# Optimization experiments

Measured on AMD Instinct MI355X. Metric: run time of the kernel, lower is better.

The kernel has to match this reference:

```python
import jax, jax.numpy as jnp
import numpy as np

N = 50000      # num nodes
E = 800000     # num edges per edge set (before self loops)
F_IN = 256     # encoding_size
F_EMB = 256    # embedding_size
PE = 98        # d2an positional features (beijing)
ALPHA1 = 0.5
ALPHA2 = 0.5


def _uniform_linear(key, out_f, in_f):
    # torch.nn.Linear default init: U(-1/sqrt(in_f), 1/sqrt(in_f))
    s = 1.0 / np.sqrt(in_f)
    return jax.random.uniform(key, (out_f, in_f), jnp.float32, -s, s)


def setup_inputs() -> dict:
    key = jax.random.key(0)
    ks = jax.random.split(key, 18)
    inp = {
        'x': jax.random.normal(ks[0], (N, F_IN), jnp.float32),
        'd2an': jax.random.normal(ks[1], (N, PE), jnp.float32),
        'edge_index_l0': jax.random.randint(ks[2], (2, E), 0, N, jnp.int32),
        'edge_attr_l0': jax.random.uniform(ks[3], (E,), jnp.float32),
        'edge_index_l1': jax.random.randint(ks[4], (2, E), 0, N, jnp.int32),
        'edge_attr_l1': jax.random.uniform(ks[5], (E,), jnp.float32),
        # nodeLin of conv1/conv2 (used only on firstLayer with usePE)
        'Wnode1': _uniform_linear(ks[6], F_IN, F_IN + PE),
        'Wnode2': _uniform_linear(ks[7], F_IN, F_IN + PE),
        # lin1/lin2 of each conv layer (bias-free linears)
        'W11': _uniform_linear(ks[8], F_EMB, F_IN),
        'W12': _uniform_linear(ks[9], F_EMB, F_IN),
        'W21': _uniform_linear(ks[10], F_EMB, F_IN),
        'W22': _uniform_linear(ks[11], F_EMB, F_IN),
        'W31': _uniform_linear(ks[12], F_EMB, F_EMB),
        'W32': _uniform_linear(ks[13], F_EMB, F_EMB),
        'W41': _uniform_linear(ks[14], F_EMB, F_EMB),
        'W42': _uniform_linear(ks[15], F_EMB, F_EMB),
    }
    return inp


def _pos_knn_gnn_layer(x, row, col, attr, d2an, Wnode, W1, W2, first):
    """PosKnnGNNLayer.forward with useSI=True, usePE=True (eval mode).

    message = deg_norm * (x_j @ W1.T) + edge_norm * (x_j @ W2.T), scatter-add to col.
    Linearity lets us aggregate (norm * x_j) first, then apply W1/W2 once per node.
    """
    n = x.shape[0]
    loop = jnp.arange(n, dtype=row.dtype)
    row = jnp.concatenate([row, loop])          # source j
    col = jnp.concatenate([col, loop])          # target i
    attr = jnp.concatenate([attr, jnp.ones((n,), attr.dtype)])  # self-loop weight 1.0

    if first:
        x = jnp.concatenate([x, d2an], axis=1) @ Wnode.T  # [n, F_IN]

    deg = jax.ops.segment_sum(jnp.ones_like(attr), col, num_segments=n)
    dinv = jnp.where(deg > 0, deg ** -0.5, 0.0)
    deg_norm = dinv[row] * dinv[col]            # [E']

    einv = jnp.where(attr > 0, attr ** -0.5, 0.0)
    edge_norm = jnp.minimum(einv, 1.0)          # clamp values > 1.0 to 1.0

    xj = x[row]                                  # gather [E', F]
    a1 = jax.ops.segment_sum(deg_norm[:, None] * xj, col, num_segments=n)
    a2 = jax.ops.segment_sum(edge_norm[:, None] * xj, col, num_segments=n)
    return a1 @ W1.T + a2 @ W2.T                 # [n, F_EMB]


def reference(x, d2an, edge_index_l0, edge_attr_l0, edge_index_l1, edge_attr_l1,
              Wnode1, Wnode2, W11, W12, W21, W22, W31, W32, W41, W42):
    r0, c0 = edge_index_l0[0], edge_index_l0[1]
    r1, c1 = edge_index_l1[0], edge_index_l1[1]

    x0 = jax.nn.relu(_pos_knn_gnn_layer(x, r0, c0, edge_attr_l0, d2an, Wnode1, W11, W12, True))
    x1 = jax.nn.relu(_pos_knn_gnn_layer(x, r1, c1, edge_attr_l1, d2an, Wnode2, W21, W22, True))
    h = ALPHA1 * x0 + ALPHA2 * x1               # dropout p=0.3 is identity in eval

    x0 = jax.nn.relu(_pos_knn_gnn_layer(h, r0, c0, edge_attr_l0, None, None, W31, W32, False))
    x1 = jax.nn.relu(_pos_knn_gnn_layer(h, r1, c1, edge_attr_l1, None, None, W41, W42, False))
    return ALPHA1 * x0 + ALPHA2 * x1
```

## Files before the change

kernel.cpp:

```cpp
#include <hip/hip_runtime.h>


using bf16x8  = __attribute__((ext_vector_type(8))) __bf16;
using floatx4 = __attribute__((ext_vector_type(4))) float;
using f32x2   = __attribute__((ext_vector_type(2))) float;

__device__ __forceinline__ float b2f(unsigned short b) {
    return __uint_as_float(((unsigned)b) << 16);
}
__device__ __forceinline__ unsigned short f2b(float f) {
    unsigned u = __float_as_uint(f);
    return (unsigned short)((u + 0x7FFFu + ((u >> 16) & 1u)) >> 16);
}
__device__ __forceinline__ unsigned short f2h(float f) {
    _Float16 h = (_Float16)f;
    return __builtin_bit_cast(unsigned short, h);
}
__device__ __forceinline__ float h2f(unsigned short u) {
    return (float)__builtin_bit_cast(_Float16, u);
}


__global__ void k_cnt2(const int* __restrict__ col0, const int* __restrict__ col1,
                       int E, int* __restrict__ cnt0, int* __restrict__ cnt1) {
    int e = blockIdx.x * 256 + threadIdx.x;
    const int* col = blockIdx.y ? col1 : col0;
    int* cnt = blockIdx.y ? cnt1 : cnt0;
    if (e < E) atomicAdd(&cnt[col[e]], 1);
}

__global__ __launch_bounds__(1024) void k_scanA(
    const int* __restrict__ cnt0, const int* __restrict__ cnt1,
    int* __restrict__ off0, int* __restrict__ off1,
    int* __restrict__ bs0, int* __restrict__ bs1, int n) {
    const int* cnt = blockIdx.y ? cnt1 : cnt0;
    int* off = blockIdx.y ? off1 : off0;
    int* bs  = blockIdx.y ? bs1 : bs0;
    __shared__ int wsum[16];
    __shared__ int wpre[16];
    const int t = threadIdx.x;
    const int lane = t & 63;
    const int w = t >> 6;
    const int i = blockIdx.x * 1024 + t;
    int v = (i < n) ? ((cnt[i] + 8) & ~7) : 0;
    #pragma unroll
    for (int d = 1; d < 64; d <<= 1) {
        int u = __shfl_up(v, d, 64);
        if (lane >= d) v += u;
    }
    if (lane == 63) wsum[w] = v;
    __syncthreads();
    if (t < 16) {
        int s2 = wsum[t];
        #pragma unroll
        for (int d = 1; d < 16; d <<= 1) {
            int u = __shfl_up(s2, d, 16);
            if (t >= d) s2 += u;
        }
        wpre[t] = s2;
    }
    __syncthreads();
    int incl = v + (w > 0 ? wpre[w - 1] : 0);
    if (i < n) off[i + 1] = incl;
    if (t == 1023) bs[blockIdx.x] = incl;
}

__global__ void k_scanB(int* __restrict__ bs0, int* __restrict__ bs1, int nb) {
    int* bs = blockIdx.y ? bs1 : bs0;
    const int t = threadIdx.x;
    int v = (t < nb) ? bs[t] : 0;
    int orig = v;
    #pragma unroll
    for (int d = 1; d < 64; d <<= 1) {
        int u = __shfl_up(v, d, 64);
        if (t >= d) v += u;
    }
    if (t < nb) bs[t] = v - orig;
}

__global__ __launch_bounds__(1024) void k_scanC(
    const int* __restrict__ bs0, const int* __restrict__ bs1,
    int* __restrict__ off0, int* __restrict__ off1, int n) {
    int* off = blockIdx.y ? off1 : off0;
    const int* bs = blockIdx.y ? bs1 : bs0;
    const int i = blockIdx.x * 1024 + threadIdx.x;
    if (i == 0) off[0] = 0;
    if (i < n && blockIdx.x > 0) off[i + 1] += bs[blockIdx.x];
}

__global__ void k_prep(const int* __restrict__ cnt0, const int* __restrict__ cnt1,
                       const int* __restrict__ off0, const int* __restrict__ off1,
                       float* __restrict__ dinv0, float* __restrict__ dinv1,
                       int* __restrict__ cur0, int* __restrict__ cur1, int n) {
    int i = blockIdx.x * 256 + threadIdx.x;
    if (i >= n) return;
    const int* cnt = blockIdx.y ? cnt1 : cnt0;
    const int* off = blockIdx.y ? off1 : off0;
    float* dinv = blockIdx.y ? dinv1 : dinv0;
    int* cur = blockIdx.y ? cur1 : cur0;
    dinv[i] = rsqrtf((float)(cnt[i] + 1));
    cur[i] = off[i];
}

__global__ void k_fill2(const int* __restrict__ ei0, const float* __restrict__ ea0,
                        const int* __restrict__ ei1, const float* __restrict__ ea1,
                        int E, const float* __restrict__ dinv0,
                        const float* __restrict__ dinv1,
                        int* __restrict__ cur0, int* __restrict__ cur1,
                        uint2* __restrict__ rec0, uint2* __restrict__ rec1) {
    int e = blockIdx.x * 256 + threadIdx.x;
    if (e >= E) return;
    const int* ei = blockIdx.y ? ei1 : ei0;
    const float* ea = blockIdx.y ? ea1 : ea0;
    const float* dinv = blockIdx.y ? dinv1 : dinv0;
    int* cur = blockIdx.y ? cur1 : cur0;
    uint2* rec = blockIdx.y ? rec1 : rec0;
    int r = ei[e];
    int c = ei[E + e];
    float a = ea[e];
    float w2 = (a > 0.0f) ? fminf(rsqrtf(a), 1.0f) : 0.0f;
    float w1 = dinv[r] * dinv[c];
    int p = atomicAdd(&cur[c], 1);
    rec[p] = make_uint2((unsigned)r,
                        ((unsigned)f2h(w1) << 16) | (unsigned)f2h(w2));
}

__global__ void k_pad(const int* __restrict__ cnt0, const int* __restrict__ cnt1,
                      const int* __restrict__ off0, const int* __restrict__ off1,
                      const float* __restrict__ dinv0, const float* __restrict__ dinv1,
                      uint2* __restrict__ rec0, uint2* __restrict__ rec1, int n) {
    int i = blockIdx.x * 256 + threadIdx.x;
    if (i >= n) return;
    const int* cnt = blockIdx.y ? cnt1 : cnt0;
    const int* off = blockIdx.y ? off1 : off0;
    const float* dinv = blockIdx.y ? dinv1 : dinv0;
    uint2* rec = blockIdx.y ? rec1 : rec0;
    int p = off[i] + cnt[i], pe = off[i + 1];
    float di = dinv[i];
    rec[p++] = make_uint2((unsigned)i,
                          ((unsigned)f2h(di * di) << 16) | 0x3C00u);
    for (; p < pe; ++p) rec[p] = make_uint2(0u, 0u);
}


__global__ void k_xc(const float* __restrict__ x, const float* __restrict__ pe,
                     unsigned short* __restrict__ xc, int n, int F, int PEd,
                     int KC, int KP) {
    int idx = blockIdx.x * 256 + threadIdx.x;
    if (idx >= n * KP) return;
    int i = idx / KP, k = idx - i * KP;
    float v = 0.0f;
    if (k < F)        v = x[(size_t)i * F + k];
    else if (k < KC)  v = pe[(size_t)i * PEd + (k - F)];
    xc[idx] = f2b(v);
}

__global__ void k_wall(const float* __restrict__ Wn1, const float* __restrict__ Wn2,
                       const float* __restrict__ W11, const float* __restrict__ W12,
                       const float* __restrict__ W21, const float* __restrict__ W22,
                       const float* __restrict__ W31, const float* __restrict__ W32,
                       const float* __restrict__ W41, const float* __restrict__ W42,
                       unsigned short* __restrict__ wn0c, unsigned short* __restrict__ wn1c,
                       unsigned short* __restrict__ wc0, unsigned short* __restrict__ wc1,
                       unsigned short* __restrict__ wc2, unsigned short* __restrict__ wc3,
                       int F, int KC, int KP) {
    int idx = blockIdx.x * 256 + threadIdx.x;
    int npad = F * KP;
    if (idx < 2 * npad) {
        const float* W = (idx < npad) ? Wn1 : Wn2;
        unsigned short* Wc = (idx < npad) ? wn0c : wn1c;
        int t = (idx < npad) ? idx : idx - npad;
        int o = t / KP, k = t - o * KP;
        Wc[t] = f2b(k < KC ? W[(size_t)o * KC + k] : 0.0f);
        return;
    }
    int t = idx - 2 * npad;
    int seg = F * 512;
    if (t >= 4 * seg) return;
    int which = t / seg;
    int r = t - which * seg;
    const float* Wa = (which == 0) ? W11 : (which == 1) ? W21 : (which == 2) ? W31 : W41;
    const float* Wb = (which == 0) ? W12 : (which == 1) ? W22 : (which == 2) ? W32 : W42;
    unsigned short* Wc = (which == 0) ? wc0 : (which == 1) ? wc1 : (which == 2) ? wc2 : wc3;
    int o = r >> 9, k = r & 511;
    float v = (k < 256) ? Wa[(size_t)o * 256 + k] : Wb[(size_t)o * 256 + (k - 256)];
    Wc[r] = f2b(v);
}


#define AGG_SLOT(g, wsel)                                                     \
    do {                                                                      \
        float w1 = h2f((unsigned short)((wsel) >> 16));                       \
        float w2 = h2f((unsigned short)((wsel) & 0xFFFFu));                   \
        f32x2 w1v = {w1, w1};                                                 \
        f32x2 w2v = {w2, w2};                                                 \
        f32x2 v;                                                              \
        v.x = __uint_as_float((g).x << 16);                                   \
        v.y = __uint_as_float((g).x & 0xFFFF0000u);                           \
        c1a = __builtin_elementwise_fma(w1v, v, c1a);                         \
        c2a = __builtin_elementwise_fma(w2v, v, c2a);                         \
        v.x = __uint_as_float((g).y << 16);                                   \
        v.y = __uint_as_float((g).y & 0xFFFF0000u);                           \
        c1b = __builtin_elementwise_fma(w1v, v, c1b);                         \
        c2b = __builtin_elementwise_fma(w2v, v, c2b);                         \
        v.x = __uint_as_float((g).z << 16);                                   \
        v.y = __uint_as_float((g).z & 0xFFFF0000u);                           \
        c1c = __builtin_elementwise_fma(w1v, v, c1c);                         \
        c2c = __builtin_elementwise_fma(w2v, v, c2c);                         \
        v.x = __uint_as_float((g).w << 16);                                   \
        v.y = __uint_as_float((g).w & 0xFFFF0000u);                           \
        c1d = __builtin_elementwise_fma(w1v, v, c1d);                         \
        c2d = __builtin_elementwise_fma(w2v, v, c2d);                         \
    } while (0)

__global__ __launch_bounds__(256) void k_agg(
    const unsigned short* __restrict__ X0, const unsigned short* __restrict__ X1,
    const int* __restrict__ off0, const int* __restrict__ off1,
    const uint2* __restrict__ rec0, const uint2* __restrict__ rec1,
    unsigned short* __restrict__ A0, unsigned short* __restrict__ A1, int n) {
    const int s = blockIdx.y;
    const char* Xb = (const char*)(s ? X1 : X0);
    const int* off = s ? off1 : off0;
    const uint2* rec = s ? rec1 : rec0;
    unsigned short* A = s ? A1 : A0;

    const int gw = (blockIdx.x * 256 + threadIdx.x) >> 6;
    const int lane = threadIdx.x & 63;
    if (gw >= n) return;

    const int e0 = __builtin_amdgcn_readfirstlane(off[gw]);
    const int e1 = __builtin_amdgcn_readfirstlane(off[gw + 1]);
    const bool hi = lane >= 32;
    const unsigned loff = (unsigned)(lane & 31) << 4;

    f32x2 c1a = {0.f, 0.f}, c1b = {0.f, 0.f}, c1c = {0.f, 0.f}, c1d = {0.f, 0.f};
    f32x2 c2a = {0.f, 0.f}, c2b = {0.f, 0.f}, c2c = {0.f, 0.f}, c2d = {0.f, 0.f};

    const uint4* recq = (const uint4*)(rec + e0);
    const int nit = (e1 - e0) >> 3;
    for (int it = 0; it < nit; ++it) {
        uint4 qa = recq[it * 4 + 0];
        uint4 qb = recq[it * 4 + 1];
        uint4 qc = recq[it * 4 + 2];
        uint4 qd = recq[it * 4 + 3];
        unsigned sa = hi ? qa.z : qa.x, wa = hi ? qa.w : qa.y;
        unsigned sb = hi ? qb.z : qb.x, wb = hi ? qb.w : qb.y;
        unsigned sc = hi ? qc.z : qc.x, wcs = hi ? qc.w : qc.y;
        unsigned sd = hi ? qd.z : qd.x, wd = hi ? qd.w : qd.y;
        uint4 ga = *(const uint4*)(Xb + ((sa << 9) | loff));
        uint4 gb = *(const uint4*)(Xb + ((sb << 9) | loff));
        uint4 gc = *(const uint4*)(Xb + ((sc << 9) | loff));
        uint4 gd = *(const uint4*)(Xb + ((sd << 9) | loff));
        AGG_SLOT(ga, wa);
        AGG_SLOT(gb, wb);
        AGG_SLOT(gc, wcs);
        AGG_SLOT(gd, wd);
    }

    float u0 = c1a.x + __shfl_xor(c1a.x, 32);
    float u1 = c1a.y + __shfl_xor(c1a.y, 32);
    float u2 = c1b.x + __shfl_xor(c1b.x, 32);
    float u3 = c1b.y + __shfl_xor(c1b.y, 32);
    float u4 = c1c.x + __shfl_xor(c1c.x, 32);
    float u5 = c1c.y + __shfl_xor(c1c.y, 32);
    float u6 = c1d.x + __shfl_xor(c1d.x, 32);
    float u7 = c1d.y + __shfl_xor(c1d.y, 32);
    float t0 = c2a.x + __shfl_xor(c2a.x, 32);
    float t1 = c2a.y + __shfl_xor(c2a.y, 32);
    float t2 = c2b.x + __shfl_xor(c2b.x, 32);
    float t3 = c2b.y + __shfl_xor(c2b.y, 32);
    float t4 = c2c.x + __shfl_xor(c2c.x, 32);
    float t5 = c2c.y + __shfl_xor(c2c.y, 32);
    float t6 = c2d.x + __shfl_xor(c2d.x, 32);
    float t7 = c2d.y + __shfl_xor(c2d.y, 32);

    float s0 = hi ? t0 : u0;
    float s1 = hi ? t1 : u1;
    float s2 = hi ? t2 : u2;
    float s3 = hi ? t3 : u3;
    float s4 = hi ? t4 : u4;
    float s5 = hi ? t5 : u5;
    float s6 = hi ? t6 : u6;
    float s7 = hi ? t7 : u7;
    uint4 o;
    o.x = (unsigned)f2b(s0) | ((unsigned)f2b(s1) << 16);
    o.y = (unsigned)f2b(s2) | ((unsigned)f2b(s3) << 16);
    o.z = (unsigned)f2b(s4) | ((unsigned)f2b(s5) << 16);
    o.w = (unsigned)f2b(s6) | ((unsigned)f2b(s7) << 16);
    *(uint4*)(A + (size_t)gw * 512 + (hi ? 256 : 0) + ((lane & 31) << 3)) = o;
}

#define GLL(g, l) \
    __builtin_amdgcn_global_load_lds((__attribute__((address_space(1))) void*)(g), \
                                     (__attribute__((address_space(3))) void*)(l), 16, 0, 0)

__global__ __launch_bounds__(256) void gemm_bt(
    const unsigned short* __restrict__ A,
    const unsigned short* __restrict__ B0, const unsigned short* __restrict__ B1,
    int M, int K, int Nc,
    unsigned short* __restrict__ outH0, unsigned short* __restrict__ outH1) {
    const unsigned short* B = blockIdx.z ? B1 : B0;
    unsigned short* outH = blockIdx.z ? outH1 : outH0;

    __shared__ __align__(16) unsigned short sA[128 * 32];
    __shared__ __align__(16) unsigned short sB[128 * 32];
    const int tid = threadIdx.x;
    const int lane = tid & 63;
    const int wave = tid >> 6;
    const int bm = blockIdx.x * 128;
    const int bn = blockIdx.y * 128;

    const int r0 = wave * 32 + (lane >> 2);
    const int kcol = (lane & 3) * 8;
    const int ga0 = min(bm + r0, M - 1);
    const int ga1 = min(bm + r0 + 16, M - 1);
    const int gb0 = min(bn + r0, Nc - 1);
    const int gb1 = min(bn + r0 + 16, Nc - 1);
    const unsigned short* pa0 = A + (size_t)ga0 * K + kcol;
    const unsigned short* pa1 = A + (size_t)ga1 * K + kcol;
    const unsigned short* pb0 = B + (size_t)gb0 * K + kcol;
    const unsigned short* pb1 = B + (size_t)gb1 * K + kcol;
    unsigned short* la0 = &sA[wave * 1024];
    unsigned short* la1 = &sA[wave * 1024 + 512];
    unsigned short* lb0 = &sB[wave * 1024];
    unsigned short* lb1 = &sB[wave * 1024 + 512];

    floatx4 acc[4][4];
    #pragma unroll
    for (int i = 0; i < 4; i++)
        #pragma unroll
        for (int j = 0; j < 4; j++) acc[i][j] = (floatx4){0.f, 0.f, 0.f, 0.f};

    const int mbase = (wave & 1) * 64 + (lane & 15);
    const int nbase = (wave >> 1) * 64 + (lane & 15);
    const int koff = (lane >> 4) * 8;

    for (int kk = 0; kk < K; kk += 32) {
        GLL(pa0 + kk, la0);
        GLL(pa1 + kk, la1);
        GLL(pb0 + kk, lb0);
        GLL(pb1 + kk, lb1);
        __syncthreads();
        bf16x8 af[4], bf[4];
        #pragma unroll
        for (int mi = 0; mi < 4; mi++)
            af[mi] = *(const bf16x8*)&sA[(mbase + mi * 16) * 32 + koff];
        #pragma unroll
        for (int ni = 0; ni < 4; ni++)
            bf[ni] = *(const bf16x8*)&sB[(nbase + ni * 16) * 32 + koff];
        #pragma unroll
        for (int mi = 0; mi < 4; mi++)
            #pragma unroll
            for (int ni = 0; ni < 4; ni++)
                acc[mi][ni] = __builtin_amdgcn_mfma_f32_16x16x32_bf16(
                    af[mi], bf[ni], acc[mi][ni], 0, 0, 0);
        __syncthreads();
    }

    const int crow = bm + (wave & 1) * 64 + (lane >> 4) * 4;
    const int ccol = bn + (wave >> 1) * 64 + (lane & 15);
    #pragma unroll
    for (int mi = 0; mi < 4; mi++)
        #pragma unroll
        for (int ni = 0; ni < 4; ni++)
            #pragma unroll
            for (int r = 0; r < 4; r++) {
                int row = crow + mi * 16 + r;
                if (row >= M) continue;
                int col = ccol + ni * 16;
                outH[(size_t)row * Nc + col] = f2b(acc[mi][ni][r]);
            }
}

__global__ __launch_bounds__(256) void gemm_dual(
    const unsigned short* __restrict__ A0, const unsigned short* __restrict__ B0,
    const unsigned short* __restrict__ A1, const unsigned short* __restrict__ B1,
    int M, int K, int Nc,
    float* __restrict__ outF, unsigned short* __restrict__ outH, float alpha) {
    __shared__ __align__(16) unsigned short sA[128 * 32];
    __shared__ __align__(16) unsigned short sB[128 * 32];
    const int tid = threadIdx.x;
    const int lane = tid & 63;
    const int wave = tid >> 6;
    const int bm = blockIdx.x * 128;
    const int bn = blockIdx.y * 128;

    const int r0 = wave * 32 + (lane >> 2);
    const int kcol = (lane & 3) * 8;
    const int ga0 = min(bm + r0, M - 1);
    const int ga1 = min(bm + r0 + 16, M - 1);
    const int gb0 = min(bn + r0, Nc - 1);
    const int gb1 = min(bn + r0 + 16, Nc - 1);
    unsigned short* la0 = &sA[wave * 1024];
    unsigned short* la1 = &sA[wave * 1024 + 512];
    unsigned short* lb0 = &sB[wave * 1024];
    unsigned short* lb1 = &sB[wave * 1024 + 512];

    const int mbase = (wave & 1) * 64 + (lane & 15);
    const int nbase = (wave >> 1) * 64 + (lane & 15);
    const int koff = (lane >> 4) * 8;

    floatx4 acc[4][4], res[4][4];

    #pragma unroll
    for (int pass = 0; pass < 2; pass++) {
        const unsigned short* A = pass ? A1 : A0;
        const unsigned short* B = pass ? B1 : B0;
        const unsigned short* pa0 = A + (size_t)ga0 * K + kcol;
        const unsigned short* pa1 = A + (size_t)ga1 * K + kcol;
        const unsigned short* pb0 = B + (size_t)gb0 * K + kcol;
        const unsigned short* pb1 = B + (size_t)gb1 * K + kcol;
        #pragma unroll
        for (int i = 0; i < 4; i++)
            #pragma unroll
            for (int j = 0; j < 4; j++) acc[i][j] = (floatx4){0.f, 0.f, 0.f, 0.f};

        for (int kk = 0; kk < K; kk += 32) {
            GLL(pa0 + kk, la0);
            GLL(pa1 + kk, la1);
            GLL(pb0 + kk, lb0);
            GLL(pb1 + kk, lb1);
            __syncthreads();
            bf16x8 af[4], bf[4];
            #pragma unroll
            for (int mi = 0; mi < 4; mi++)
                af[mi] = *(const bf16x8*)&sA[(mbase + mi * 16) * 32 + koff];
            #pragma unroll
            for (int ni = 0; ni < 4; ni++)
                bf[ni] = *(const bf16x8*)&sB[(nbase + ni * 16) * 32 + koff];
            #pragma unroll
            for (int mi = 0; mi < 4; mi++)
                #pragma unroll
                for (int ni = 0; ni < 4; ni++)
                    acc[mi][ni] = __builtin_amdgcn_mfma_f32_16x16x32_bf16(
                        af[mi], bf[ni], acc[mi][ni], 0, 0, 0);
            __syncthreads();
        }
        if (pass == 0) {
            #pragma unroll
            for (int mi = 0; mi < 4; mi++)
                #pragma unroll
                for (int ni = 0; ni < 4; ni++)
                    #pragma unroll
                    for (int r = 0; r < 4; r++)
                        res[mi][ni][r] = fmaxf(acc[mi][ni][r], 0.0f);
        }
    }

    const int crow = bm + (wave & 1) * 64 + (lane >> 4) * 4;
    const int ccol = bn + (wave >> 1) * 64 + (lane & 15);
    #pragma unroll
    for (int mi = 0; mi < 4; mi++)
        #pragma unroll
        for (int ni = 0; ni < 4; ni++)
            #pragma unroll
            for (int r = 0; r < 4; r++) {
                int row = crow + mi * 16 + r;
                if (row >= M) continue;
                int col = ccol + ni * 16;
                float v = alpha * (res[mi][ni][r] + fmaxf(acc[mi][ni][r], 0.0f));
                size_t idx = (size_t)row * Nc + col;
                if (outF) outF[idx] = v;
                else      outH[idx] = f2b(v);
            }
}


extern "C" void kernel_launch(void* const* d_in, const int* in_sizes, int n_in,
                              void* d_out, int out_size, void* d_ws, size_t ws_size,
                              hipStream_t stream) {
    const int F = 256;
    const int N = in_sizes[0] / F;
    const int PEd = in_sizes[1] / N;
    const int E = in_sizes[2] / 2;
    const int KC = F + PEd;
    const int KP = (KC + 31) & ~31;

    const float* x   = (const float*)d_in[0];
    const float* pe  = (const float*)d_in[1];
    const int*   ei0 = (const int*)d_in[2];
    const float* ea0 = (const float*)d_in[3];
    const int*   ei1 = (const int*)d_in[4];
    const float* ea1 = (const float*)d_in[5];
    const float* Wn1 = (const float*)d_in[6];
    const float* Wn2 = (const float*)d_in[7];
    const float* W11 = (const float*)d_in[8];
    const float* W12 = (const float*)d_in[9];
    const float* W21 = (const float*)d_in[10];
    const float* W22 = (const float*)d_in[11];
    const float* W31 = (const float*)d_in[12];
    const float* W32 = (const float*)d_in[13];
    const float* W41 = (const float*)d_in[14];
    const float* W42 = (const float*)d_in[15];
    float* out = (float*)d_out;

    char* p = (char*)d_ws;
    auto alloc = [&](size_t b) -> char* {
        char* r = p;
        p += (b + 255) & ~(size_t)255;
        return r;
    };
    int*   cnt0  = (int*)alloc((size_t)N * 4);
    int*   cnt1  = (int*)alloc((size_t)N * 4);
    int*   off0  = (int*)alloc((size_t)(N + 1) * 4);
    int*   off1  = (int*)alloc((size_t)(N + 1) * 4);
    int*   cur0  = (int*)alloc((size_t)N * 4);
    int*   cur1  = (int*)alloc((size_t)N * 4);
    float* dinv0 = (float*)alloc((size_t)N * 4);
    float* dinv1 = (float*)alloc((size_t)N * 4);
    int*   bs0   = (int*)alloc(64 * 4);
    int*   bs1   = (int*)alloc(64 * 4);
    uint2* rec0  = (uint2*)alloc(((size_t)E + 8ull * N) * 8);
    uint2* rec1  = (uint2*)alloc(((size_t)E + 8ull * N) * 8);
    unsigned short* wn0c = (unsigned short*)alloc((size_t)F * KP * 2);
    unsigned short* wn1c = (unsigned short*)alloc((size_t)F * KP * 2);
    unsigned short* wc0  = (unsigned short*)alloc((size_t)F * 512 * 2);
    unsigned short* wc1  = (unsigned short*)alloc((size_t)F * 512 * 2);
    unsigned short* wc2  = (unsigned short*)alloc((size_t)F * 512 * 2);
    unsigned short* wc3  = (unsigned short*)alloc((size_t)F * 512 * 2);
    unsigned short* xa   = (unsigned short*)alloc((size_t)N * 512 * 2);
    unsigned short* xb   = xa + (size_t)N * 256;
    unsigned short* h    = (unsigned short*)alloc((size_t)N * F * 2);
    unsigned short* a12  = (unsigned short*)alloc((size_t)N * 512 * 2);
    unsigned short* xc   = a12;
    unsigned short* a12bL1 = (unsigned short*)d_out;
    unsigned short* a12bL2 = xa;

    const int B = 256;
    const int gE = (E + B - 1) / B;
    const int gN = (N + B - 1) / B;
    const int gW = (N + 3) / 4;
    const int nb = (N + 1023) / 1024;
    dim3 gemm_grid((N + 127) / 128, 2);
    dim3 gemm_grid2((N + 127) / 128, 2, 2);

    hipMemsetAsync(cnt0, 0, (size_t)N * 4, stream);
    hipMemsetAsync(cnt1, 0, (size_t)N * 4, stream);
    k_cnt2<<<dim3(gE, 2), B, 0, stream>>>(ei0 + E, ei1 + E, E, cnt0, cnt1);
    k_scanA<<<dim3(nb, 2), 1024, 0, stream>>>(cnt0, cnt1, off0, off1, bs0, bs1, N);
    k_scanB<<<dim3(1, 2), 64, 0, stream>>>(bs0, bs1, nb);
    k_scanC<<<dim3(nb, 2), 1024, 0, stream>>>(bs0, bs1, off0, off1, N);
    k_prep<<<dim3(gN, 2), B, 0, stream>>>(cnt0, cnt1, off0, off1, dinv0, dinv1, cur0, cur1, N);
    k_fill2<<<dim3(gE, 2), B, 0, stream>>>(ei0, ea0, ei1, ea1, E, dinv0, dinv1,
                                           cur0, cur1, rec0, rec1);
    k_pad<<<dim3(gN, 2), B, 0, stream>>>(cnt0, cnt1, off0, off1, dinv0, dinv1,
                                         rec0, rec1, N);

    k_xc<<<((size_t)N * KP + B - 1) / B, B, 0, stream>>>(x, pe, xc, N, F, PEd, KC, KP);
    {
        int tot = 2 * F * KP + 4 * F * 512;
        k_wall<<<(tot + B - 1) / B, B, 0, stream>>>(Wn1, Wn2, W11, W12, W21, W22,
                                                    W31, W32, W41, W42,
                                                    wn0c, wn1c, wc0, wc1, wc2, wc3,
                                                    F, KC, KP);
    }

    gemm_bt<<<gemm_grid2, B, 0, stream>>>(xc, wn0c, wn1c, N, KP, F, xa, xb);

    k_agg<<<dim3(gW, 2), B, 0, stream>>>(xa, xb, off0, off1, rec0, rec1,
                                         a12, a12bL1, N);
    gemm_dual<<<gemm_grid, B, 0, stream>>>(a12, wc0, a12bL1, wc1, N, 512, F,
                                           nullptr, h, 0.5f);

    k_agg<<<dim3(gW, 2), B, 0, stream>>>(h, h, off0, off1, rec0, rec1,
                                         a12, a12bL2, N);
    gemm_dual<<<gemm_grid, B, 0, stream>>>(a12, wc2, a12bL2, wc3, N, 512, F,
                                           out, nullptr, 0.5f);
}
```

Measured before the change: 756.4 us.

## Fuse CSR prep kernels, vectorize input conversion, software-pipeline aggregation gathers

Folds the dinv/cursor computation into the scan-finalize kernel and merges edge fill with self-loop padding into one launch, cutting several small kernel launches. The cursor is now derived from the padded end offset rather than the start offset. Input concatenation and bf16 conversion now handles 8 elements per thread with float4 loads and uint4 stores. The aggregation loop prefetches the next group's records and feature rows before doing the FMAs, which overlaps gather latency with arithmetic at the cost of more registers.

```diff
diff --git a/kernel.cpp b/kernel.cpp
--- a/kernel.cpp
+++ b/kernel.cpp
@@ -5,9 +5,6 @@
 using floatx4 = __attribute__((ext_vector_type(4))) float;
 using f32x2   = __attribute__((ext_vector_type(2))) float;
 
-__device__ __forceinline__ float b2f(unsigned short b) {
-    return __uint_as_float(((unsigned)b) << 16);
-}
 __device__ __forceinline__ unsigned short f2b(float f) {
     unsigned u = __float_as_uint(f);
     return (unsigned short)((u + 0x7FFFu + ((u >> 16) & 1u)) >> 16);
@@ -80,79 +77,103 @@
 
 __global__ __launch_bounds__(1024) void k_scanC(
     const int* __restrict__ bs0, const int* __restrict__ bs1,
-    int* __restrict__ off0, int* __restrict__ off1, int n) {
+    const int* __restrict__ cnt0, const int* __restrict__ cnt1,
+    int* __restrict__ off0, int* __restrict__ off1,
+    float* __restrict__ dinv0, float* __restrict__ dinv1,
+    int* __restrict__ cur0, int* __restrict__ cur1, int n) {
     int* off = blockIdx.y ? off1 : off0;
     const int* bs = blockIdx.y ? bs1 : bs0;
+    const int* cnt = blockIdx.y ? cnt1 : cnt0;
+    float* dinv = blockIdx.y ? dinv1 : dinv0;
+    int* cur = blockIdx.y ? cur1 : cur0;
     const int i = blockIdx.x * 1024 + threadIdx.x;
     if (i == 0) off[0] = 0;
-    if (i < n && blockIdx.x > 0) off[i + 1] += bs[blockIdx.x];
-}
-
-__global__ void k_prep(const int* __restrict__ cnt0, const int* __restrict__ cnt1,
-                       const int* __restrict__ off0, const int* __restrict__ off1,
-                       float* __restrict__ dinv0, float* __restrict__ dinv1,
-                       int* __restrict__ cur0, int* __restrict__ cur1, int n) {
-    int i = blockIdx.x * 256 + threadIdx.x;
-    if (i >= n) return;
-    const int* cnt = blockIdx.y ? cnt1 : cnt0;
-    const int* off = blockIdx.y ? off1 : off0;
-    float* dinv = blockIdx.y ? dinv1 : dinv0;
-    int* cur = blockIdx.y ? cur1 : cur0;
-    dinv[i] = rsqrtf((float)(cnt[i] + 1));
-    cur[i] = off[i];
-}
-
-__global__ void k_fill2(const int* __restrict__ ei0, const float* __restrict__ ea0,
-                        const int* __restrict__ ei1, const float* __restrict__ ea1,
-                        int E, const float* __restrict__ dinv0,
-                        const float* __restrict__ dinv1,
-                        int* __restrict__ cur0, int* __restrict__ cur1,
-                        uint2* __restrict__ rec0, uint2* __restrict__ rec1) {
-    int e = blockIdx.x * 256 + threadIdx.x;
-    if (e >= E) return;
-    const int* ei = blockIdx.y ? ei1 : ei0;
-    const float* ea = blockIdx.y ? ea1 : ea0;
-    const float* dinv = blockIdx.y ? dinv1 : dinv0;
-    int* cur = blockIdx.y ? cur1 : cur0;
-    uint2* rec = blockIdx.y ? rec1 : rec0;
-    int r = ei[e];
-    int c = ei[E + e];
-    float a = ea[e];
-    float w2 = (a > 0.0f) ? fminf(rsqrtf(a), 1.0f) : 0.0f;
-    float w1 = dinv[r] * dinv[c];
-    int p = atomicAdd(&cur[c], 1);
-    rec[p] = make_uint2((unsigned)r,
-                        ((unsigned)f2h(w1) << 16) | (unsigned)f2h(w2));
-}
-
-__global__ void k_pad(const int* __restrict__ cnt0, const int* __restrict__ cnt1,
-                      const int* __restrict__ off0, const int* __restrict__ off1,
-                      const float* __restrict__ dinv0, const float* __restrict__ dinv1,
-                      uint2* __restrict__ rec0, uint2* __restrict__ rec1, int n) {
-    int i = blockIdx.x * 256 + threadIdx.x;
-    if (i >= n) return;
-    const int* cnt = blockIdx.y ? cnt1 : cnt0;
-    const int* off = blockIdx.y ? off1 : off0;
-    const float* dinv = blockIdx.y ? dinv1 : dinv0;
-    uint2* rec = blockIdx.y ? rec1 : rec0;
-    int p = off[i] + cnt[i], pe = off[i + 1];
-    float di = dinv[i];
-    rec[p++] = make_uint2((unsigned)i,
-                          ((unsigned)f2h(di * di) << 16) | 0x3C00u);
-    for (; p < pe; ++p) rec[p] = make_uint2(0u, 0u);
-}
-
-
-__global__ void k_xc(const float* __restrict__ x, const float* __restrict__ pe,
-                     unsigned short* __restrict__ xc, int n, int F, int PEd,
-                     int KC, int KP) {
+    if (i < n) {
+        int ci = cnt[i];
+        int o = off[i + 1] + (blockIdx.x > 0 ? bs[blockIdx.x] : 0);
+        off[i + 1] = o;
+        cur[i] = o - ((ci + 8) & ~7);
+        dinv[i] = rsqrtf((float)(ci + 1));
+    }
+}
+
+__global__ void k_fillpad(
+    const int* __restrict__ ei0, const float* __restrict__ ea0,
+    const int* __restrict__ ei1, const float* __restrict__ ea1,
+    int E, int EB,
+    const int* __restrict__ cnt0, const int* __restrict__ cnt1,
+    const int* __restrict__ off0, const int* __restrict__ off1,
+    const float* __restrict__ dinv0, const float* __restrict__ dinv1,
+    int* __restrict__ cur0, int* __restrict__ cur1,
+    uint2* __restrict__ rec0, uint2* __restrict__ rec1, int n) {
+    const int s = blockIdx.y;
+    const float* dinv = s ? dinv1 : dinv0;
+    uint2* rec = s ? rec1 : rec0;
+    int t = blockIdx.x * 256 + threadIdx.x;
+    if (t < EB) {
+        int e = t;
+        if (e >= E) return;
+        const int* ei = s ? ei1 : ei0;
+        const float* ea = s ? ea1 : ea0;
+        int* cur = s ? cur1 : cur0;
+        int r = ei[e];
+        int c = ei[E + e];
+        float a = ea[e];
+        float w2 = (a > 0.0f) ? fminf(rsqrtf(a), 1.0f) : 0.0f;
+        float w1 = dinv[r] * dinv[c];
+        int p = atomicAdd(&cur[c], 1);
+        rec[p] = make_uint2((unsigned)r,
+                            ((unsigned)f2h(w1) << 16) | (unsigned)f2h(w2));
+    } else {
+        int i = t - EB;
+        if (i >= n) return;
+        const int* cnt = s ? cnt1 : cnt0;
+        const int* off = s ? off1 : off0;
+        int p = off[i] + cnt[i], pe = off[i + 1];
+        float di = dinv[i];
+        rec[p++] = make_uint2((unsigned)i,
+                              ((unsigned)f2h(di * di) << 16) | 0x3C00u);
+        for (; p < pe; ++p) rec[p] = make_uint2(0u, 0u);
+    }
+}
+
+
+__global__ void k_xcv(const float* __restrict__ x, const float* __restrict__ pe,
+                      unsigned short* __restrict__ xc, int n, int F, int PEd,
+                      int KC, int KP) {
+    const int CH = KP >> 3;
     int idx = blockIdx.x * 256 + threadIdx.x;
-    if (idx >= n * KP) return;
-    int i = idx / KP, k = idx - i * KP;
-    float v = 0.0f;
-    if (k < F)        v = x[(size_t)i * F + k];
-    else if (k < KC)  v = pe[(size_t)i * PEd + (k - F)];
-    xc[idx] = f2b(v);
+    if (idx >= n * CH) return;
+    int i = idx / CH, c = idx - i * CH;
+    int k = c << 3;
+    uint4 o;
+    if (k + 8 <= F) {
+        const float4* px = (const float4*)(x + (size_t)i * F + k);
+        float4 v0 = px[0];
+        float4 v1 = px[1];
+        o.x = (unsigned)f2b(v0.x) | ((unsigned)f2b(v0.y) << 16);
+        o.y = (unsigned)f2b(v0.z) | ((unsigned)f2b(v0.w) << 16);
+        o.z = (unsigned)f2b(v1.x) | ((unsigned)f2b(v1.y) << 16);
+        o.w = (unsigned)f2b(v1.z) | ((unsigned)f2b(v1.w) << 16);
+    } else if (k < KC) {
+        const float* pp = pe + (size_t)i * PEd + (k - F);
+        int rem = KC - k;
+        float e0 = pp[0];
+        float e1 = (1 < rem) ? pp[1] : 0.f;
+        float e2 = (2 < rem) ? pp[2] : 0.f;
+        float e3 = (3 < rem) ? pp[3] : 0.f;
+        float e4 = (4 < rem) ? pp[4] : 0.f;
+        float e5 = (5 < rem) ? pp[5] : 0.f;
+        float e6 = (6 < rem) ? pp[6] : 0.f;
+        float e7 = (7 < rem) ? pp[7] : 0.f;
+        o.x = (unsigned)f2b(e0) | ((unsigned)f2b(e1) << 16);
+        o.y = (unsigned)f2b(e2) | ((unsigned)f2b(e3) << 16);
+        o.z = (unsigned)f2b(e4) | ((unsigned)f2b(e5) << 16);
+        o.w = (unsigned)f2b(e6) | ((unsigned)f2b(e7) << 16);
+    } else {
+        o.x = o.y = o.z = o.w = 0u;
+    }
+    *(uint4*)(xc + (size_t)idx * 8) = o;
 }
 
 __global__ void k_wall(const float* __restrict__ Wn1, const float* __restrict__ Wn2,
@@ -213,6 +234,13 @@
         c2d = __builtin_elementwise_fma(w2v, v, c2d);                         \
     } while (0)
 
+#define SELG(q, wsel, g)                                                      \
+    do {                                                                      \
+        unsigned _s = hi ? (q).z : (q).x;                                     \
+        wsel = hi ? (q).w : (q).y;                                            \
+        g = *(const uint4*)(Xb + ((_s << 9) | loff));                         \
+    } while (0)
+
 __global__ __launch_bounds__(256) void k_agg(
     const unsigned short* __restrict__ X0, const unsigned short* __restrict__ X1,
     const int* __restrict__ off0, const int* __restrict__ off1,
@@ -238,24 +266,36 @@
 
     const uint4* recq = (const uint4*)(rec + e0);
     const int nit = (e1 - e0) >> 3;
-    for (int it = 0; it < nit; ++it) {
-        uint4 qa = recq[it * 4 + 0];
-        uint4 qb = recq[it * 4 + 1];
-        uint4 qc = recq[it * 4 + 2];
-        uint4 qd = recq[it * 4 + 3];
-        unsigned sa = hi ? qa.z : qa.x, wa = hi ? qa.w : qa.y;
-        unsigned sb = hi ? qb.z : qb.x, wb = hi ? qb.w : qb.y;
-        unsigned sc = hi ? qc.z : qc.x, wcs = hi ? qc.w : qc.y;
-        unsigned sd = hi ? qd.z : qd.x, wd = hi ? qd.w : qd.y;
-        uint4 ga = *(const uint4*)(Xb + ((sa << 9) | loff));
-        uint4 gb = *(const uint4*)(Xb + ((sb << 9) | loff));
-        uint4 gc = *(const uint4*)(Xb + ((sc << 9) | loff));
-        uint4 gd = *(const uint4*)(Xb + ((sd << 9) | loff));
+
+    uint4 qa = recq[0], qb = recq[1], qc = recq[2], qd = recq[3];
+    unsigned wa, wb, wcs, wd;
+    uint4 ga, gb, gc, gd;
+    SELG(qa, wa, ga);
+    SELG(qb, wb, gb);
+    SELG(qc, wcs, gc);
+    SELG(qd, wd, gd);
+
+    #pragma unroll 2
+    for (int it = 0; it < nit - 1; ++it) {
+        const uint4* nq = recq + (size_t)(it + 1) * 4;
+        uint4 na = nq[0], nb = nq[1], nc = nq[2], nd = nq[3];
+        unsigned nwa, nwb, nwc, nwd;
+        uint4 nga, ngb, ngc, ngd;
+        SELG(na, nwa, nga);
+        SELG(nb, nwb, ngb);
+        SELG(nc, nwc, ngc);
+        SELG(nd, nwd, ngd);
         AGG_SLOT(ga, wa);
         AGG_SLOT(gb, wb);
         AGG_SLOT(gc, wcs);
         AGG_SLOT(gd, wd);
-    }
+        wa = nwa; wb = nwb; wcs = nwc; wd = nwd;
+        ga = nga; gb = ngb; gc = ngc; gd = ngd;
+    }
+    AGG_SLOT(ga, wa);
+    AGG_SLOT(gb, wb);
+    AGG_SLOT(gc, wcs);
+    AGG_SLOT(gd, wd);
 
     float u0 = c1a.x + __shfl_xor(c1a.x, 32);
     float u1 = c1a.y + __shfl_xor(c1a.y, 32);
@@ -539,14 +579,14 @@
     k_cnt2<<<dim3(gE, 2), B, 0, stream>>>(ei0 + E, ei1 + E, E, cnt0, cnt1);
     k_scanA<<<dim3(nb, 2), 1024, 0, stream>>>(cnt0, cnt1, off0, off1, bs0, bs1, N);
     k_scanB<<<dim3(1, 2), 64, 0, stream>>>(bs0, bs1, nb);
-    k_scanC<<<dim3(nb, 2), 1024, 0, stream>>>(bs0, bs1, off0, off1, N);
-    k_prep<<<dim3(gN, 2), B, 0, stream>>>(cnt0, cnt1, off0, off1, dinv0, dinv1, cur0, cur1, N);
-    k_fill2<<<dim3(gE, 2), B, 0, stream>>>(ei0, ea0, ei1, ea1, E, dinv0, dinv1,
-                                           cur0, cur1, rec0, rec1);
-    k_pad<<<dim3(gN, 2), B, 0, stream>>>(cnt0, cnt1, off0, off1, dinv0, dinv1,
-                                         rec0, rec1, N);
-
-    k_xc<<<((size_t)N * KP + B - 1) / B, B, 0, stream>>>(x, pe, xc, N, F, PEd, KC, KP);
+    k_scanC<<<dim3(nb, 2), 1024, 0, stream>>>(bs0, bs1, cnt0, cnt1, off0, off1,
+                                              dinv0, dinv1, cur0, cur1, N);
+    k_fillpad<<<dim3(gE + gN, 2), B, 0, stream>>>(
+        ei0, ea0, ei1, ea1, E, gE * B, cnt0, cnt1, off0, off1,
+        dinv0, dinv1, cur0, cur1, rec0, rec1, N);
+
+    k_xcv<<<((size_t)N * (KP / 8) + B - 1) / B, B, 0, stream>>>(
+        x, pe, xc, N, F, PEd, KC, KP);
     {
         int tot = 2 * F * KP + 4 * F * 512;
         k_wall<<<(tot + B - 1) / B, B, 0, stream>>>(Wn1, Wn2, W11, W12, W21, W22,
```

Result: faster. 725.5 us (-4.1%).
